# Kernel tuning notes

Hardware: AMD Instinct MI355X
Metric: run time of the kernel (lower is better)

## Reference

```python
import jax, jax.numpy as jnp
import numpy as np

EXTENT = 1.0  # influence radius of kernel points (init arg `extent`)
N = 100000    # number of input points
M = 100000    # number of output points
NN = 32       # neighbors per output point
K = 15        # kernel points
F = 64        # input feature channels
C = 64        # output channels


def setup_inputs() -> dict:
    key = jax.random.key(0)
    k1, k2, k3, k4, k5, k6 = jax.random.split(key, 6)
    points = jax.random.normal(k1, (N, 3), dtype=jnp.float32)
    features = jax.random.normal(k2, (N, F), dtype=jnp.float32)
    output_points = jax.random.normal(k3, (M, 3), dtype=jnp.float32)
    neighbor_indices = jax.random.randint(k4, (M, NN), 0, N, dtype=jnp.int32)
    # kernel point positions within ~1.5*extent ball (load_kernels surrogate)
    k_points = jax.random.normal(k5, (K, 3), dtype=jnp.float32) * 0.5
    k_values = jax.random.normal(k6, (K, F, C), dtype=jnp.float32) * 0.05
    return {
        "points": points,
        "features": features,
        "output_points": output_points,
        "neighbor_indices": neighbor_indices,
        "k_points": k_points,
        "k_values": k_values,
    }


def reference(points, features, output_points, neighbor_indices, k_points, k_values):
    # gather neighbor coordinates and features: [M, NN, 3], [M, NN, F]
    nbr_pts = points[neighbor_indices]
    nbr_feat = features[neighbor_indices]
    # relative position of each neighbor to each kernel point: [M, NN, K, 3]
    diff = nbr_pts[:, :, None, :] - output_points[:, None, None, :] - k_points[None, None, :, :]
    sq_dist = jnp.sum(diff * diff, axis=-1)                 # [M, NN, K]
    # linear influence weights
    w = jnp.maximum(1.0 - jnp.sqrt(sq_dist) / EXTENT, 0.0)  # [M, NN, K]
    # weighted sum over neighbors -> [K, M, F] (avoids materializing [M,NN,K,F])
    wf = jnp.einsum('mnk,mnf->kmf', w, nbr_feat)
    # per-kernel-point matmul then sum over kernel points -> [M, C]
    out = jnp.einsum('kmf,kfc->mc', wf, k_values)
    return out
```

## Files before the change

### kernel.cpp

```cpp
#include <hip/hip_runtime.h>

typedef short bf16x8 __attribute__((ext_vector_type(8)));
typedef float f32x4 __attribute__((ext_vector_type(4)));
typedef unsigned int u32;
typedef unsigned short u16;

__device__ __forceinline__ u16 f2bf(float x) {
  union { float f; u32 u; } v; v.f = x;
  u32 r = (v.u + 0x7fffu + ((v.u >> 16) & 1u)) >> 16;
  return (u16)r;
}
__device__ __forceinline__ u32 pk2(float a, float b) {
  return (u32)f2bf(a) | ((u32)f2bf(b) << 16);
}

__global__ void feat_cvt(const float* __restrict__ src, u16* __restrict__ dst, int n4) {
  int i = blockIdx.x * 256 + threadIdx.x;
  if (i < n4) {
    float4 v = ((const float4*)src)[i];
    ushort4 o;
    o.x = f2bf(v.x); o.y = f2bf(v.y); o.z = f2bf(v.z); o.w = f2bf(v.w);
    ((ushort4*)dst)[i] = o;
  }
}

__global__ void kv_stage(const float* __restrict__ kv, u16* __restrict__ kvb) {
  int t = blockIdx.x * 256 + threadIdx.x;
  int l = t & 63;
  int tile = t >> 6;
  int ct2 = tile & 3, sb = tile >> 2;
  int c = ct2 * 16 + (l & 15);
  u32 q[4];
#pragma unroll
  for (int jp = 0; jp < 4; ++jp) {
    u16 vv[2];
#pragma unroll
    for (int h = 0; h < 2; ++h) {
      int j = jp * 2 + h;
      int idx = sb * 32 + 8 * (l >> 4) + j;
      int reg  = idx & 3;
      int ctlo = (idx >> 2) & 1;
      int fl   = (idx >> 3) & 15;
      int kh   = (idx >> 7) & 3;
      int cthi = (idx >> 9) & 1;
      int kp = kh * 4 + reg;
      int f  = (cthi * 2 + ctlo) * 16 + fl;
      float val = (kp < 15) ? kv[(kp * 64 + f) * 64 + c] : 0.f;
      vv[h] = f2bf(val);
    }
    q[jp] = (u32)vv[0] | ((u32)vv[1] << 16);
  }
  ((uint4*)kvb)[t] = make_uint4(q[0], q[1], q[2], q[3]);
}

__global__ __launch_bounds__(256, 3) void kpconv_main(
    const float* __restrict__ points,
    const float* __restrict__ outpts,
    const int*   __restrict__ nbr,
    const u16*   __restrict__ featg,
    const u16*   __restrict__ kvb,
    const float* __restrict__ kpts,
    float* __restrict__ out, int M)
{
  __shared__ __align__(16) u16 featB[4][2048];
  __shared__ __align__(16) u16 wfs[16 * 1024];
  __shared__ float npx[4][32], npy[4][32], npz[4][32];
  __shared__ int nidx[4][32];

  const int tid = threadIdx.x;
  const int w = tid >> 6;
  const int l = tid & 63;
  const int khi = l >> 4, flo = l & 15;
  const int mbase = blockIdx.x * 16;

  float kx = 0.f, ky = 0.f, kz = 0.f;
  if (flo < 15) { kx = kpts[flo*3+0]; ky = kpts[flo*3+1]; kz = kpts[flo*3+2]; }

  const f32x4 zero = {0.f,0.f,0.f,0.f};

  for (int t = 0; t < 4; ++t) {
    int mi = w * 4 + t;
    int m0 = mbase + mi;
    bool mvalid = m0 < M;
    int m = mvalid ? m0 : (M - 1);

    if (l < 32) {
      int id = nbr[m * 32 + l];
      nidx[w][l] = id;
      npx[w][l] = points[id*3+0]; npy[w][l] = points[id*3+1]; npz[w][l] = points[id*3+2];
    }
    float ox = outpts[m*3+0], oy = outpts[m*3+1], oz = outpts[m*3+2];
    asm volatile("s_waitcnt lgkmcnt(0)" ::: "memory");
    __builtin_amdgcn_wave_barrier();

#pragma unroll
    for (int a = 0; a < 4; ++a) {
      u32 p[4];
#pragma unroll
      for (int jp = 0; jp < 4; ++jp) {
        u16 v0 = featg[(u32)nidx[w][8*a + 2*jp + 0] * 64u + (u32)l];
        u16 v1 = featg[(u32)nidx[w][8*a + 2*jp + 1] * 64u + (u32)l];
        p[jp] = (u32)v0 | ((u32)v1 << 16);
      }
      *(uint4*)&featB[w][khi*512 + a*128 + flo*8] = make_uint4(p[0], p[1], p[2], p[3]);
    }
    asm volatile("s_waitcnt lgkmcnt(0)" ::: "memory");
    __builtin_amdgcn_wave_barrier();

    bf16x8 aw;
#pragma unroll
    for (int j = 0; j < 8; ++j) {
      int n = 8*khi + j;
      float dx = npx[w][n] - ox - kx;
      float dy = npy[w][n] - oy - ky;
      float dz = npz[w][n] - oz - kz;
      float wt = 1.f - sqrtf(dx*dx + dy*dy + dz*dz);
      wt = (flo < 15 && mvalid) ? fmaxf(wt, 0.f) : 0.f;
      aw[j] = (short)f2bf(wt);
    }

    f32x4 wf0 = __builtin_amdgcn_mfma_f32_16x16x32_bf16(aw, *(bf16x8*)&featB[w][0*512 + l*8], zero, 0,0,0);
    f32x4 wf1 = __builtin_amdgcn_mfma_f32_16x16x32_bf16(aw, *(bf16x8*)&featB[w][1*512 + l*8], zero, 0,0,0);
    f32x4 wf2 = __builtin_amdgcn_mfma_f32_16x16x32_bf16(aw, *(bf16x8*)&featB[w][2*512 + l*8], zero, 0,0,0);
    f32x4 wf3 = __builtin_amdgcn_mfma_f32_16x16x32_bf16(aw, *(bf16x8*)&featB[w][3*512 + l*8], zero, 0,0,0);

    uint4 s0 = make_uint4(pk2(wf0[0],wf0[1]), pk2(wf0[2],wf0[3]), pk2(wf1[0],wf1[1]), pk2(wf1[2],wf1[3]));
    uint4 s1 = make_uint4(pk2(wf2[0],wf2[1]), pk2(wf2[2],wf2[3]), pk2(wf3[0],wf3[1]), pk2(wf3[2],wf3[3]));
    u32 b0 = (u32)(mi*2048 + l*16) ^ ((u32)(mi & 7) << 4);
    *(uint4*)((char*)wfs + b0)          = s0;
    *(uint4*)((char*)wfs + (b0 + 1024)) = s1;
  }
  __syncthreads();

  f32x4 acc = {0.f,0.f,0.f,0.f};
  for (int sb = 0; sb < 32; ++sb) {
    u32 ra = (u32)(flo*2048 + sb*64 + khi*16) ^ ((u32)(flo & 7) << 4);
    bf16x8 af = *(bf16x8*)((char*)wfs + ra);
    const u16* kb = kvb + (u32)((sb*4 + w)*64 + l) * 8u;
    acc = __builtin_amdgcn_mfma_f32_16x16x32_bf16(af, *(const bf16x8*)kb, acc, 0,0,0);
  }

#pragma unroll
  for (int r = 0; r < 4; ++r) {
    int m = mbase + 4*khi + r;
    if (m < M) {
      out[(u32)m * 64u + (u32)(w*16 + flo)] = acc[r];
    }
  }
}

extern "C" void kernel_launch(void* const* d_in, const int* in_sizes, int n_in,
                              void* d_out, int out_size, void* d_ws, size_t ws_size,
                              hipStream_t stream) {
  const float* points   = (const float*)d_in[0];
  const float* features = (const float*)d_in[1];
  const float* outpts   = (const float*)d_in[2];
  const int*   nbridx   = (const int*)d_in[3];
  const float* kpts     = (const float*)d_in[4];
  const float* kvals    = (const float*)d_in[5];
  float* out = (float*)d_out;

  int N = in_sizes[0] / 3;
  int M = in_sizes[2] / 3;

  u16* featg = (u16*)d_ws;
  u16* kvb   = (u16*)((char*)d_ws + (size_t)N * 64 * 2);

  int n4 = (N * 64) / 4;
  feat_cvt<<<(n4 + 255) / 256, 256, 0, stream>>>(features, featg, n4);
  kv_stage<<<32, 256, 0, stream>>>(kvals, kvb);
  kpconv_main<<<(M + 15) / 16, 256, 0, stream>>>(points, outpts, nbridx, featg, kvb, kpts, out, M);
}
```

Baseline: 209.9 us.

## Halve wf LDS staging buffer with two-phase contraction to raise occupancy

The shared wf buffer drops from 32KB to 16KB. The second half of each row's wf results is kept in registers during the first contraction pass, then written into the reused buffer for a second pass. Launch bounds go from 3 to 4 blocks per SM, allowing more resident blocks to hide gather latency. The cost is two extra block-wide barriers, more live registers, and serialised contraction phases.

```diff
diff --git a/kernel.cpp b/kernel.cpp
--- a/kernel.cpp
+++ b/kernel.cpp
@@ -53,7 +53,7 @@
   ((uint4*)kvb)[t] = make_uint4(q[0], q[1], q[2], q[3]);
 }
 
-__global__ __launch_bounds__(256, 3) void kpconv_main(
+__global__ __launch_bounds__(256, 4) void kpconv_main(
     const float* __restrict__ points,
     const float* __restrict__ outpts,
     const int*   __restrict__ nbr,
@@ -63,7 +63,7 @@
     float* __restrict__ out, int M)
 {
   __shared__ __align__(16) u16 featB[4][2048];
-  __shared__ __align__(16) u16 wfs[16 * 1024];
+  __shared__ __align__(16) u16 wfs[16 * 512];
   __shared__ float npx[4][32], npy[4][32], npz[4][32];
   __shared__ int nidx[4][32];
 
@@ -77,6 +77,7 @@
   if (flo < 15) { kx = kpts[flo*3+0]; ky = kpts[flo*3+1]; kz = kpts[flo*3+2]; }
 
   const f32x4 zero = {0.f,0.f,0.f,0.f};
+  uint4 sreg0, sreg1, sreg2, sreg3;
 
   for (int t = 0; t < 4; ++t) {
     int mi = w * 4 + t;
@@ -126,26 +127,44 @@
 
     uint4 s0 = make_uint4(pk2(wf0[0],wf0[1]), pk2(wf0[2],wf0[3]), pk2(wf1[0],wf1[1]), pk2(wf1[2],wf1[3]));
     uint4 s1 = make_uint4(pk2(wf2[0],wf2[1]), pk2(wf2[2],wf2[3]), pk2(wf3[0],wf3[1]), pk2(wf3[2],wf3[3]));
-    u32 b0 = (u32)(mi*2048 + l*16) ^ ((u32)(mi & 7) << 4);
-    *(uint4*)((char*)wfs + b0)          = s0;
-    *(uint4*)((char*)wfs + (b0 + 1024)) = s1;
+    u32 b0 = (u32)(mi*1024 + l*16) ^ ((u32)(mi & 7) << 4);
+    *(uint4*)((char*)wfs + b0) = s0;
+    if      (t == 0) sreg0 = s1;
+    else if (t == 1) sreg1 = s1;
+    else if (t == 2) sreg2 = s1;
+    else             sreg3 = s1;
   }
   __syncthreads();
 
   f32x4 acc = {0.f,0.f,0.f,0.f};
-  for (int sb = 0; sb < 32; ++sb) {
-    u32 ra = (u32)(flo*2048 + sb*64 + khi*16) ^ ((u32)(flo & 7) << 4);
-    bf16x8 af = *(bf16x8*)((char*)wfs + ra);
-    const u16* kb = kvb + (u32)((sb*4 + w)*64 + l) * 8u;
+  for (int sbl = 0; sbl < 16; ++sbl) {
+    u32 ra = (u32)(flo*1024) + (((u32)(sbl*64 + khi*16)) ^ ((u32)(flo & 7) << 4));
+    bf16x8 af = *(const bf16x8*)((char*)wfs + ra);
+    const u16* kb = kvb + (u32)((sbl*4 + w)*64 + l) * 8u;
+    acc = __builtin_amdgcn_mfma_f32_16x16x32_bf16(af, *(const bf16x8*)kb, acc, 0,0,0);
+  }
+  __syncthreads();
+
+#pragma unroll
+  for (int t = 0; t < 4; ++t) {
+    int mi = w*4 + t;
+    u32 b0 = (u32)(mi*1024 + l*16) ^ ((u32)(mi & 7) << 4);
+    uint4 sv = (t==0) ? sreg0 : (t==1) ? sreg1 : (t==2) ? sreg2 : sreg3;
+    *(uint4*)((char*)wfs + b0) = sv;
+  }
+  __syncthreads();
+
+  for (int sbl = 0; sbl < 16; ++sbl) {
+    u32 ra = (u32)(flo*1024) + (((u32)(sbl*64 + khi*16)) ^ ((u32)(flo & 7) << 4));
+    bf16x8 af = *(const bf16x8*)((char*)wfs + ra);
+    const u16* kb = kvb + (u32)(((16 + sbl)*4 + w)*64 + l) * 8u;
     acc = __builtin_amdgcn_mfma_f32_16x16x32_bf16(af, *(const bf16x8*)kb, acc, 0,0,0);
   }
 
 #pragma unroll
   for (int r = 0; r < 4; ++r) {
     int m = mbase + 4*khi + r;
-    if (m < M) {
-      out[(u32)m * 64u + (u32)(w*16 + flo)] = acc[r];
-    }
+    if (m < M) out[(size_t)m * 64 + (u32)(w*16 + flo)] = acc[r];
   }
 }
 
```

Result: slower. 214.1 us (+2.0%).
